# Performance work log

Hardware: AMD Instinct MI355X
Metric: run time of the kernel (lower is better)

Reference implementation:

```python
import jax, jax.numpy as jnp
import numpy as np

# ---- problem constants (mirror AdjustInstanceArea __init__ args) ----
NUM_NODES = 2_000_000
NUM_MOVABLE = 1_500_000
NUM_FILLER = 400_000
NUM_NETS = 1_500_000
PINS_PER_NET = 4                       # uniform netpin_start = arange(0, P+1, 4)
NUM_PINS = NUM_NETS * PINS_PER_NET
XL, XH, YL, YH = 0.0, 1000.0, 0.0, 1000.0
NBX = NBY = 512
BIN_W = (XH - XL) / NBX
BIN_H = (YH - YL) / NBY
UNIT_H_CAP = 1.5                       # unit horizontal routing capacity
UNIT_V_CAP = 1.5                       # unit vertical routing capacity
MAX_RATE = 2.0                         # max_route_opt_adjust_rate
MIN_RATE = 1.0 / MAX_RATE
EPS = 1e-6


def setup_inputs() -> dict:
    key = jax.random.key(0)
    k = jax.random.split(key, 4)
    x = jax.random.uniform(k[0], (NUM_NODES,), jnp.float32, XL, XH - 4.0)
    y = jax.random.uniform(k[1], (NUM_NODES,), jnp.float32, YL, YH - 4.0)
    pos = jnp.concatenate([x, y])                      # [2*num_nodes], x then y

    # pins clustered around net centers (realistic small net bboxes)
    rng = np.random.default_rng(0)
    centers = rng.uniform(0.0, 1000.0, size=(NUM_NETS, 1, 2)).astype(np.float32)
    jit = rng.uniform(-20.0, 20.0, size=(NUM_NETS, PINS_PER_NET, 2)).astype(np.float32)
    ppos = np.clip(centers + jit, 0.0, 1000.0)         # [nets, pins_per_net, 2], in net order

    # flat_netpin: pin ids grouped by net; pin_pos indexed by pin id
    flat_netpin = rng.permutation(NUM_PINS).astype(np.int32)
    px = np.empty(NUM_PINS, np.float32); py = np.empty(NUM_PINS, np.float32)
    px[flat_netpin] = ppos[..., 0].reshape(-1)
    py[flat_netpin] = ppos[..., 1].reshape(-1)
    pin_pos = jnp.concatenate([jnp.asarray(px), jnp.asarray(py)])  # [2*num_pins]

    pin2net = jnp.asarray(np.repeat(np.arange(NUM_NETS, dtype=np.int32), PINS_PER_NET))

    node_size_x = jax.random.uniform(k[2], (NUM_NODES,), jnp.float32, 1.0, 4.0)
    node_size_y = jax.random.uniform(k[3], (NUM_NODES,), jnp.float32, 1.0, 4.0)
    return {"pos": pos, "pin_pos": pin_pos,
            "node_size_x": node_size_x, "node_size_y": node_size_y,
            "flat_netpin": jnp.asarray(flat_netpin), "pin2net": pin2net}


def _rect_accum(vals, blx, bly, bhx, bhy):
    """Accumulate vals over inclusive bin rectangles via difference map + 2D cumsum."""
    D = jnp.zeros((NBX + 1, NBY + 1), vals.dtype)
    D = D.at[blx, bly].add(vals)
    D = D.at[bhx + 1, bly].add(-vals)
    D = D.at[blx, bhy + 1].add(-vals)
    D = D.at[bhx + 1, bhy + 1].add(vals)
    return jnp.cumsum(jnp.cumsum(D, axis=0), axis=1)[:NBX, :NBY]


def reference(pos, pin_pos, node_size_x, node_size_y, flat_netpin, pin2net):
    # ---- InstanceRouteOptimizationArea: RUDY routing demand per bin ----
    px = pin_pos[:NUM_PINS][flat_netpin].reshape(NUM_NETS, PINS_PER_NET)
    py = pin_pos[NUM_PINS:][flat_netpin].reshape(NUM_NETS, PINS_PER_NET)
    net_xl = jnp.min(px, axis=1); net_xh = jnp.max(px, axis=1)
    net_yl = jnp.min(py, axis=1); net_yh = jnp.max(py, axis=1)
    bw = net_xh - net_xl
    bh = net_yh - net_yl
    barea = jnp.maximum(bw * bh, EPS)
    dens_h = bw / barea                                # horizontal wire density
    dens_v = bh / barea                                # vertical wire density

    blx = jnp.clip(jnp.floor((net_xl - XL) / BIN_W), 0, NBX - 1).astype(jnp.int32)
    bhx = jnp.clip(jnp.floor((net_xh - XL) / BIN_W), 0, NBX - 1).astype(jnp.int32)
    bly = jnp.clip(jnp.floor((net_yl - YL) / BIN_H), 0, NBY - 1).astype(jnp.int32)
    bhy = jnp.clip(jnp.floor((net_yh - YL) / BIN_H), 0, NBY - 1).astype(jnp.int32)

    util_h = _rect_accum(dens_h, blx, bly, bhx, bhy) / UNIT_H_CAP
    util_v = _rect_accum(dens_v, blx, bly, bhx, bhy) / UNIT_V_CAP

    # per-movable-node utilization (gather at node center bin)
    x = pos[:NUM_NODES]; y = pos[NUM_NODES:]
    nsx_m = node_size_x[:NUM_MOVABLE]; nsy_m = node_size_y[:NUM_MOVABLE]
    cx = x[:NUM_MOVABLE] + 0.5 * nsx_m
    cy = y[:NUM_MOVABLE] + 0.5 * nsy_m
    bix = jnp.clip(jnp.floor((cx - XL) / BIN_W), 0, NBX - 1).astype(jnp.int32)
    biy = jnp.clip(jnp.floor((cy - YL) / BIN_H), 0, NBY - 1).astype(jnp.int32)
    util = jnp.maximum(util_h[bix, biy], util_v[bix, biy])
    ratio = jnp.clip(util, MIN_RATE, MAX_RATE)

    area_old = nsx_m * nsy_m
    instance_route_area = area_old * ratio

    # ---- AdjustInstanceArea: rescale under max_total_area budget ----
    filler_area_old = jnp.sum(node_size_x[NUM_NODES - NUM_FILLER:] *
                              node_size_y[NUM_NODES - NUM_FILLER:])
    max_total_area = jnp.sum(area_old) + filler_area_old
    scale = jnp.minimum(1.0, max_total_area / jnp.maximum(jnp.sum(instance_route_area), EPS))
    new_area = instance_route_area * scale
    sr = jnp.sqrt(new_area / jnp.maximum(area_old, EPS))
    nsx_new = nsx_m * sr
    nsy_new = nsy_m * sr

    # keep cell centers fixed while resizing
    x_out = x.at[:NUM_MOVABLE].add(0.5 * (nsx_m - nsx_new))
    y_out = y.at[:NUM_MOVABLE].add(0.5 * (nsy_m - nsy_new))

    # fillers absorb leftover area budget
    fscale = jnp.sqrt(jnp.maximum(max_total_area - jnp.sum(new_area), 0.0) /
                      jnp.maximum(filler_area_old, EPS))
    nsx_out = node_size_x.at[:NUM_MOVABLE].set(nsx_new)
    nsx_out = nsx_out.at[NUM_NODES - NUM_FILLER:].multiply(fscale)
    nsy_out = node_size_y.at[:NUM_MOVABLE].set(nsy_new)
    nsy_out = nsy_out.at[NUM_NODES - NUM_FILLER:].multiply(fscale)

    return jnp.concatenate([x_out, y_out, nsx_out, nsy_out])  # [4*num_nodes]
```

## Files before the change

kernel.cpp:

```cpp
#include <hip/hip_runtime.h>
#include <hip/hip_fp16.h>
#include <math.h>

#define N_NODES   2000000
#define N_MOVABLE 1500000
#define N_FILLER  400000
#define N_NETS    1500000
#define N_PINS    (N_NETS * 4)
#define NB        512
#define NT        16
#define TILE      32
#define NBUCKET   (NT * NT)
#define CAP       10240
#define NSLICE    4
#define NMAPS     NSLICE
#define RED_BLOCKS 1024

#define NQ        24
#define QRNG      250000
#define NXCD      8
#define RPX       3
#define PIN_PER_XCD (QRNG * RPX)
#define P2CHUNK   4096
#define P2CHUNKS  ((PIN_PER_XCD + P2CHUNK - 1) / P2CHUNK)

__device__ __forceinline__ int bin_idx(float v) {
    float b = floorf(v / 1.953125f);
    b = fminf(fmaxf(b, 0.0f), 511.0f);
    return (int)b;
}

__global__ __launch_bounds__(1024)
void p1_bucketq_kernel(const int* __restrict__ fnp,
                       uint2* __restrict__ qslab,
                       unsigned* __restrict__ g_qptr) {
    __shared__ unsigned hist[NQ];
    __shared__ unsigned hbase[NQ];
    int t = threadIdx.x;
    if (t < NQ) hist[t] = 0;
    __syncthreads();

    int s0 = blockIdx.x * 4096 + t * 4;
    unsigned q[4]; unsigned qb[4]; unsigned rk[4]; bool val[4];
    if (s0 + 3 < N_PINS) {
        int4 f = *reinterpret_cast<const int4*>(fnp + s0);
        q[0] = (unsigned)f.x; q[1] = (unsigned)f.y;
        q[2] = (unsigned)f.z; q[3] = (unsigned)f.w;
        val[0] = val[1] = val[2] = val[3] = true;
    } else {
        #pragma unroll
        for (int j = 0; j < 4; ++j) {
            val[j] = (s0 + j < N_PINS);
            q[j] = val[j] ? (unsigned)fnp[s0 + j] : 0u;
        }
    }
    #pragma unroll
    for (int j = 0; j < 4; ++j) {
        qb[j] = q[j] / (unsigned)QRNG;
        rk[j] = val[j] ? atomicAdd(&hist[qb[j]], 1u) : 0u;
    }
    __syncthreads();
    if (t < NQ) {
        unsigned c = hist[t];
        hbase[t] = c ? atomicAdd(&g_qptr[t], c) : 0u;
    }
    __syncthreads();
    #pragma unroll
    for (int j = 0; j < 4; ++j) {
        if (val[j]) {
            unsigned idx = qb[j] * (unsigned)QRNG + hbase[qb[j]] + rk[j];
            qslab[idx] = make_uint2(q[j], (unsigned)(s0 + j));
        }
    }
}

__global__ __launch_bounds__(1024)
void p2_gather_kernel(const uint2* __restrict__ qslab,
                      const float* __restrict__ pin_pos,
                      unsigned* __restrict__ sxy) {
    unsigned k = blockIdx.x & (NXCD - 1);
    unsigned c = blockIdx.x >> 3;
    unsigned t = threadIdx.x;
    #pragma unroll
    for (int j = 0; j < 4; ++j) {
        unsigned s = c * (unsigned)P2CHUNK + t + (unsigned)j * 1024u;
        if (s < (unsigned)PIN_PER_XCD) {
            unsigned rl = s / (unsigned)QRNG;
            unsigned ridx = s - rl * (unsigned)QRNG;
            uint2 qr = qslab[(k + 8u * rl) * (unsigned)QRNG + ridx];
            float x = pin_pos[qr.x];
            float y = pin_pos[qr.x + N_PINS];
            unsigned xq = __float2uint_rn(x * 64.0f);
            unsigned yq = __float2uint_rn(y * 64.0f);
            sxy[qr.y] = xq | (yq << 16);
        }
    }
}

__device__ __forceinline__ uint2 pack_tile_rec(float bw, float bh,
                                               unsigned blx, unsigned bhx,
                                               unsigned bly, unsigned bhy,
                                               int* tb) {
    float barea = fmaxf(bw * bh, 1e-6f);
    float vh = fminf((bw / barea) * (1.0f / 1.5f), 60000.0f);
    float vv = fminf((bh / barea) * (1.0f / 1.5f), 60000.0f);
    *tb = (int)((bly >> 5) * NT + (blx >> 5));
    __half2 h = __float22half2_rn(make_float2(vh, vv));
    uint2 r;
    r.x = *reinterpret_cast<unsigned*>(&h);
    r.y = blx | (bly << 9) | ((bhx + 1 - blx) << 18) | ((bhy + 1 - bly) << 23);
    return r;
}

__global__ __launch_bounds__(1024)
void p3_netrec_kernel(const unsigned* __restrict__ sxy,
                      uint2* __restrict__ tslab,
                      unsigned* __restrict__ g_tptr) {
    __shared__ unsigned hist[NBUCKET];
    __shared__ unsigned hbase[NBUCKET];
    int t = threadIdx.x;
    if (t < NBUCKET) hist[t] = 0;
    __syncthreads();

    int n0 = blockIdx.x * 4096 + t;
    uint2 rec[4]; int tb[4]; unsigned rk[4];
    #pragma unroll
    for (int u = 0; u < 4; ++u) {
        int n = n0 + u * 1024;
        tb[u] = -1;
        if (n < N_NETS) {
            uint4 v = *reinterpret_cast<const uint4*>(sxy + 4 * (size_t)n);
            unsigned x0 = v.x & 0xffffu, y0 = v.x >> 16;
            unsigned x1 = v.y & 0xffffu, y1 = v.y >> 16;
            unsigned x2 = v.z & 0xffffu, y2 = v.z >> 16;
            unsigned x3 = v.w & 0xffffu, y3 = v.w >> 16;
            unsigned xl = min(min(x0, x1), min(x2, x3));
            unsigned xh = max(max(x0, x1), max(x2, x3));
            unsigned yl = min(min(y0, y1), min(y2, y3));
            unsigned yh = max(max(y0, y1), max(y2, y3));
            float bw = (float)(xh - xl) * 0.015625f;
            float bh = (float)(yh - yl) * 0.015625f;
            unsigned blx = min(xl / 125u, 511u), bhx = min(xh / 125u, 511u);
            unsigned bly = min(yl / 125u, 511u), bhy = min(yh / 125u, 511u);
            rec[u] = pack_tile_rec(bw, bh, blx, bhx, bly, bhy, &tb[u]);
            rk[u] = atomicAdd(&hist[tb[u]], 1u);
        }
    }
    __syncthreads();
    if (t < NBUCKET) {
        unsigned c = hist[t];
        hbase[t] = c ? atomicAdd(&g_tptr[t], c) : 0u;
    }
    __syncthreads();
    #pragma unroll
    for (int u = 0; u < 4; ++u) {
        if (tb[u] >= 0) {
            unsigned s = hbase[tb[u]] + rk[u];
            if (s < CAP) tslab[(size_t)tb[u] * CAP + s] = rec[u];
        }
    }
}

__global__ void pack_kernel(const float* __restrict__ pin_pos,
                            float2* __restrict__ pp) {
    int i = blockIdx.x * blockDim.x + threadIdx.x;
    if (i >= N_PINS / 4) return;
    float4 a = reinterpret_cast<const float4*>(pin_pos)[i];
    float4 b = reinterpret_cast<const float4*>(pin_pos + N_PINS)[i];
    float4* o = reinterpret_cast<float4*>(pp + 4 * (size_t)i);
    o[0] = make_float4(a.x, b.x, a.y, b.y);
    o[1] = make_float4(a.z, b.z, a.w, b.w);
}

template <bool PACKED>
__device__ __forceinline__ uint2 make_rec_f(const float* __restrict__ pin_pos,
                                            const float2* __restrict__ pp,
                                            int4 fp, int* tb) {
    float2 p0, p1, p2, p3;
    if (PACKED) {
        p0 = pp[fp.x]; p1 = pp[fp.y]; p2 = pp[fp.z]; p3 = pp[fp.w];
    } else {
        p0 = make_float2(pin_pos[fp.x], pin_pos[N_PINS + fp.x]);
        p1 = make_float2(pin_pos[fp.y], pin_pos[N_PINS + fp.y]);
        p2 = make_float2(pin_pos[fp.z], pin_pos[N_PINS + fp.z]);
        p3 = make_float2(pin_pos[fp.w], pin_pos[N_PINS + fp.w]);
    }
    float xl = fminf(fminf(p0.x, p1.x), fminf(p2.x, p3.x));
    float xh = fmaxf(fmaxf(p0.x, p1.x), fmaxf(p2.x, p3.x));
    float yl = fminf(fminf(p0.y, p1.y), fminf(p2.y, p3.y));
    float yh = fmaxf(fmaxf(p0.y, p1.y), fmaxf(p2.y, p3.y));
    unsigned blx = bin_idx(xl), bhx = bin_idx(xh);
    unsigned bly = bin_idx(yl), bhy = bin_idx(yh);
    return pack_tile_rec(xh - xl, yh - yl, blx, bhx, bly, bhy, tb);
}

template <bool PACKED>
__global__ __launch_bounds__(1024)
void gather_bin_kernel(const float* __restrict__ pin_pos,
                       const float2* __restrict__ pp,
                       const int* __restrict__ fnp,
                       uint2* __restrict__ slab,
                       unsigned* __restrict__ g_ptr) {
    __shared__ unsigned hist[NBUCKET];
    __shared__ unsigned hbase[NBUCKET];
    int t = threadIdx.x;
    if (t < NBUCKET) hist[t] = 0;
    __syncthreads();

    int n0 = blockIdx.x * 4096 + t;
    bool v[4]; int4 fp[4]; uint2 r[4]; int b[4]; unsigned rk[4];
    #pragma unroll
    for (int k = 0; k < 4; ++k) {
        int n = n0 + k * 1024;
        v[k] = (n < N_NETS);
        fp[k] = v[k] ? *reinterpret_cast<const int4*>(fnp + 4 * (size_t)n)
                     : make_int4(0, 0, 0, 0);
    }
    #pragma unroll
    for (int k = 0; k < 4; ++k) {
        b[k] = 0;
        if (v[k]) r[k] = make_rec_f<PACKED>(pin_pos, pp, fp[k], &b[k]);
    }
    #pragma unroll
    for (int k = 0; k < 4; ++k) rk[k] = v[k] ? atomicAdd(&hist[b[k]], 1u) : 0u;
    __syncthreads();
    if (t < NBUCKET) {
        unsigned c = hist[t];
        hbase[t] = c ? atomicAdd(&g_ptr[t], c) : 0u;
    }
    __syncthreads();
    #pragma unroll
    for (int k = 0; k < 4; ++k) {
        if (v[k]) {
            unsigned s = hbase[b[k]] + rk[k];
            if (s < CAP) slab[(size_t)b[k] * CAP + s] = r[k];
        }
    }
}

__device__ __forceinline__ void rec_process(uint2 r, int x0, int y0,
                                            float2* acc) {
    float2 v = __half22float2(*reinterpret_cast<const __half2*>(&r.x));
    unsigned g = r.y;
    int ax0 = (int)(g & 511u);
    int ay0 = (int)((g >> 9) & 511u);
    int ax1 = ax0 + (int)((g >> 18) & 31u);
    int ay1 = ay0 + (int)((g >> 23) & 31u);
    int X0 = ax0 - x0, Y0 = ay0 - y0;
    int X1 = ax1 - x0, Y1 = ay1 - y0;
    bool iX0 = (unsigned)X0 < TILE, iX1 = (unsigned)X1 < TILE;
    bool iY0 = (unsigned)Y0 < TILE, iY1 = (unsigned)Y1 < TILE;
    if (iX0 && iY0) { atomicAdd(&acc[X0 * TILE + Y0].x,  v.x); atomicAdd(&acc[X0 * TILE + Y0].y,  v.y); }
    if (iX1 && iY0) { atomicAdd(&acc[X1 * TILE + Y0].x, -v.x); atomicAdd(&acc[X1 * TILE + Y0].y, -v.y); }
    if (iX0 && iY1) { atomicAdd(&acc[X0 * TILE + Y1].x, -v.x); atomicAdd(&acc[X0 * TILE + Y1].y, -v.y); }
    if (iX1 && iY1) { atomicAdd(&acc[X1 * TILE + Y1].x,  v.x); atomicAdd(&acc[X1 * TILE + Y1].y,  v.y); }
}

__global__ __launch_bounds__(256)
void accum_kernel(const uint2* __restrict__ slab,
                  const unsigned* __restrict__ g_cnt,
                  float2* __restrict__ Dp) {
    __shared__ float2 acc[TILE * TILE];
    int wg = blockIdx.x;
    int sl = wg & (NSLICE - 1), tile = wg >> 2;
    int tx = tile & (NT - 1), ty = tile >> 4;
    int tid = threadIdx.x;

    for (int i = tid; i < TILE * TILE; i += 256) acc[i] = make_float2(0.f, 0.f);
    __syncthreads();

    int x0 = tx * TILE, y0 = ty * TILE;
    #pragma unroll
    for (int dy = -1; dy <= 0; ++dy) {
        int sy = ty + dy; if (sy < 0) continue;
        #pragma unroll
        for (int dx = -1; dx <= 0; ++dx) {
            int sx = tx + dx; if (sx < 0) continue;
            int sb = sy * NT + sx;
            unsigned cnt = min(g_cnt[sb], (unsigned)CAP);
            unsigned lo = (cnt * (unsigned)sl) >> 2;
            unsigned hi = (cnt * (unsigned)(sl + 1)) >> 2;
            const uint2* recs = slab + (size_t)sb * CAP;
            unsigned i = lo + tid;
            for (; i + 768 < hi; i += 1024) {
                uint2 r0 = recs[i];
                uint2 r1 = recs[i + 256];
                uint2 r2 = recs[i + 512];
                uint2 r3 = recs[i + 768];
                rec_process(r0, x0, y0, acc);
                rec_process(r1, x0, y0, acc);
                rec_process(r2, x0, y0, acc);
                rec_process(r3, x0, y0, acc);
            }
            for (; i < hi; i += 256) rec_process(recs[i], x0, y0, acc);
        }
    }
    __syncthreads();

    float2* D = Dp + (size_t)sl * NB * NB;
    for (int i = tid; i < TILE * TILE; i += 256) {
        int X = i >> 5, Y = i & 31;
        D[(size_t)(x0 + X) * NB + (y0 + Y)] = acc[i];
    }
}

__global__ __launch_bounds__(512)
void scanA_kernel(const float2* __restrict__ Dp, float2* __restrict__ S) {
    __shared__ float2 s[NB];
    int x = blockIdx.x, t = threadIdx.x;
    float2 a = make_float2(0.f, 0.f);
    #pragma unroll
    for (int m = 0; m < NMAPS; ++m) {
        float2 v = Dp[(size_t)m * NB * NB + (size_t)x * NB + t];
        a.x += v.x; a.y += v.y;
    }
    s[t] = a;
    __syncthreads();
    for (int off = 1; off < NB; off <<= 1) {
        float2 u = s[t];
        if (t >= off) { float2 w = s[t - off]; u.x += w.x; u.y += w.y; }
        __syncthreads();
        s[t] = u;
        __syncthreads();
    }
    S[(size_t)x * NB + t] = s[t];
}

__global__ __launch_bounds__(512)
void scanB_kernel(float2* __restrict__ S) {
    __shared__ float2 s[NB];
    int y = blockIdx.x, t = threadIdx.x;
    s[t] = S[(size_t)t * NB + y];
    __syncthreads();
    for (int off = 1; off < NB; off <<= 1) {
        float2 u = s[t];
        if (t >= off) { float2 w = s[t - off]; u.x += w.x; u.y += w.y; }
        __syncthreads();
        s[t] = u;
        __syncthreads();
    }
    S[(size_t)t * NB + y] = s[t];
}

__global__ __launch_bounds__(256)
void reduce_kernel(const float* __restrict__ pos,
                   const float* __restrict__ nsx,
                   const float* __restrict__ nsy,
                   const float2* __restrict__ S,
                   double* __restrict__ partials) {
    const int MQ = N_MOVABLE / 4;
    const int TQ = MQ + N_FILLER / 4;
    double a_old = 0.0, a_route = 0.0, a_fill = 0.0;
    int stride = gridDim.x * blockDim.x;
    for (int q = blockIdx.x * blockDim.x + threadIdx.x; q < TQ; q += stride) {
        if (q < MQ) {
            int i = 4 * q;
            float4 x4  = *reinterpret_cast<const float4*>(pos + i);
            float4 y4  = *reinterpret_cast<const float4*>(pos + N_NODES + i);
            float4 sx4 = *reinterpret_cast<const float4*>(nsx + i);
            float4 sy4 = *reinterpret_cast<const float4*>(nsy + i);
            float xs[4] = {x4.x, x4.y, x4.z, x4.w};
            float ys[4] = {y4.x, y4.y, y4.z, y4.w};
            float sxs[4] = {sx4.x, sx4.y, sx4.z, sx4.w};
            float sys[4] = {sy4.x, sy4.y, sy4.z, sy4.w};
            #pragma unroll
            for (int k = 0; k < 4; ++k) {
                int bx = bin_idx(xs[k] + 0.5f * sxs[k]);
                int by = bin_idx(ys[k] + 0.5f * sys[k]);
                float2 u2 = S[(size_t)bx * NB + by];
                float ratio = fminf(fmaxf(fmaxf(u2.x, u2.y), 0.5f), 2.0f);
                float area = sxs[k] * sys[k];
                a_old += (double)area;
                a_route += (double)(area * ratio);
            }
        } else {
            int j = (N_NODES - N_FILLER) + 4 * (q - MQ);
            float4 sx4 = *reinterpret_cast<const float4*>(nsx + j);
            float4 sy4 = *reinterpret_cast<const float4*>(nsy + j);
            a_fill += (double)(sx4.x * sy4.x + sx4.y * sy4.y +
                               sx4.z * sy4.z + sx4.w * sy4.w);
        }
    }
    for (int off = 32; off > 0; off >>= 1) {
        a_old   += __shfl_down(a_old, off);
        a_route += __shfl_down(a_route, off);
        a_fill  += __shfl_down(a_fill, off);
    }
    __shared__ double sd[4][3];
    int wid = threadIdx.x >> 6, lane = threadIdx.x & 63;
    if (lane == 0) { sd[wid][0] = a_old; sd[wid][1] = a_route; sd[wid][2] = a_fill; }
    __syncthreads();
    if (threadIdx.x == 0) {
        double s0 = 0, s1 = 0, s2 = 0;
        for (int w = 0; w < 4; ++w) { s0 += sd[w][0]; s1 += sd[w][1]; s2 += sd[w][2]; }
        partials[blockIdx.x * 3 + 0] = s0;
        partials[blockIdx.x * 3 + 1] = s1;
        partials[blockIdx.x * 3 + 2] = s2;
    }
}

__global__ __launch_bounds__(256)
void finish_kernel(const double* __restrict__ partials,
                   double* __restrict__ sums) {
    int t = threadIdx.x;
    double s0 = 0, s1 = 0, s2 = 0;
    for (int r = t; r < RED_BLOCKS; r += 256) {
        s0 += partials[r * 3 + 0];
        s1 += partials[r * 3 + 1];
        s2 += partials[r * 3 + 2];
    }
    for (int off = 32; off > 0; off >>= 1) {
        s0 += __shfl_down(s0, off);
        s1 += __shfl_down(s1, off);
        s2 += __shfl_down(s2, off);
    }
    __shared__ double sd[4][3];
    int wid = t >> 6, lane = t & 63;
    if (lane == 0) { sd[wid][0] = s0; sd[wid][1] = s1; sd[wid][2] = s2; }
    __syncthreads();
    if (t == 0) {
        double a = 0, b = 0, c = 0;
        for (int w = 0; w < 4; ++w) { a += sd[w][0]; b += sd[w][1]; c += sd[w][2]; }
        sums[0] = a; sums[1] = b; sums[2] = c;
    }
}

__global__ __launch_bounds__(256)
void final_kernel(const float* __restrict__ pos,
                  const float* __restrict__ nsx,
                  const float* __restrict__ nsy,
                  const float2* __restrict__ S,
                  const double* __restrict__ sums,
                  float* __restrict__ out) {
    double sum_area  = sums[0];
    double sum_route = sums[1];
    double fill_old  = sums[2];
    double max_total = sum_area + fill_old;

    float scale = fminf(1.0f, (float)(max_total / fmax(sum_route, 1e-6)));
    float sum_new = (float)(scale * (float)sum_route);
    float fscale = sqrtf(fmaxf((float)max_total - sum_new, 0.0f) /
                         fmaxf((float)fill_old, 1e-6f));

    int q = blockIdx.x * blockDim.x + threadIdx.x;
    if (q >= N_NODES / 4) return;
    int i = 4 * q;

    float4 x4  = *reinterpret_cast<const float4*>(pos + i);
    float4 y4  = *reinterpret_cast<const float4*>(pos + N_NODES + i);
    float4 sx4 = *reinterpret_cast<const float4*>(nsx + i);
    float4 sy4 = *reinterpret_cast<const float4*>(nsy + i);

    float xs[4] = {x4.x, x4.y, x4.z, x4.w};
    float ys[4] = {y4.x, y4.y, y4.z, y4.w};
    float sxs[4] = {sx4.x, sx4.y, sx4.z, sx4.w};
    float sys[4] = {sy4.x, sy4.y, sy4.z, sy4.w};

    if (i < N_MOVABLE) {
        #pragma unroll
        for (int k = 0; k < 4; ++k) {
            int bx = bin_idx(xs[k] + 0.5f * sxs[k]);
            int by = bin_idx(ys[k] + 0.5f * sys[k]);
            float2 u2 = S[(size_t)bx * NB + by];
            float ratio = fminf(fmaxf(fmaxf(u2.x, u2.y), 0.5f), 2.0f);
            float area = sxs[k] * sys[k];
            float new_area = area * ratio * scale;
            float sr = sqrtf(new_area / fmaxf(area, 1e-6f));
            float sx_new = sxs[k] * sr, sy_new = sys[k] * sr;
            xs[k] = xs[k] + 0.5f * (sxs[k] - sx_new);
            ys[k] = ys[k] + 0.5f * (sys[k] - sy_new);
            sxs[k] = sx_new; sys[k] = sy_new;
        }
    } else if (i >= N_NODES - N_FILLER) {
        #pragma unroll
        for (int k = 0; k < 4; ++k) { sxs[k] *= fscale; sys[k] *= fscale; }
    }

    *reinterpret_cast<float4*>(out + i)               = make_float4(xs[0], xs[1], xs[2], xs[3]);
    *reinterpret_cast<float4*>(out + N_NODES + i)     = make_float4(ys[0], ys[1], ys[2], ys[3]);
    *reinterpret_cast<float4*>(out + 2 * N_NODES + i) = make_float4(sxs[0], sxs[1], sxs[2], sxs[3]);
    *reinterpret_cast<float4*>(out + 3 * N_NODES + i) = make_float4(sys[0], sys[1], sys[2], sys[3]);
}

extern "C" void kernel_launch(void* const* d_in, const int* in_sizes, int n_in,
                              void* d_out, int out_size, void* d_ws, size_t ws_size,
                              hipStream_t stream) {
    const float* pos         = (const float*)d_in[0];
    const float* pin_pos     = (const float*)d_in[1];
    const float* nsx         = (const float*)d_in[2];
    const float* nsy         = (const float*)d_in[3];
    const int*   flat_netpin = (const int*)d_in[4];
    float* out = (float*)d_out;

    const size_t qslab_b = (size_t)N_PINS * sizeof(uint2);
    const size_t sxy_b   = (size_t)N_PINS * sizeof(unsigned);
    const size_t tslab_b = (size_t)NBUCKET * CAP * sizeof(uint2);
    const size_t ctr_b   = 4096;
    const size_t dp_b    = (size_t)NMAPS * NB * NB * sizeof(float2);
    const size_t s_b     = (size_t)NB * NB * sizeof(float2);
    const size_t part_b  = (size_t)RED_BLOCKS * 3 * sizeof(double);
    const size_t pp_b    = (size_t)N_PINS * sizeof(float2);

    const size_t need_new = qslab_b + sxy_b + tslab_b + ctr_b;
    const size_t need_r8  = pp_b + tslab_b + ctr_b;

    char* base = (char*)d_ws;
    int tier = (ws_size >= need_new) ? 0 : (ws_size >= need_r8) ? 1 : 2;

    uint2* tslab; unsigned* ctrs; float2* Dp; float2* S;
    double* partials; double* sums;

    if (tier == 0) {
        uint2*    qslab = (uint2*)base;
        unsigned* sxy   = (unsigned*)(base + qslab_b);
        tslab           = (uint2*)(base + qslab_b + sxy_b);
        ctrs            = (unsigned*)(base + qslab_b + sxy_b + tslab_b);
        Dp       = (float2*)base;
        S        = (float2*)(base + dp_b);
        partials = (double*)(base + dp_b + s_b);
        sums     = (double*)(base + dp_b + s_b + part_b);

        unsigned* g_qptr = ctrs;
        unsigned* g_tptr = ctrs + 448;

        hipMemsetAsync(ctrs, 0, ctr_b, stream);
        p1_bucketq_kernel<<<(N_PINS + 4095) / 4096, 1024, 0, stream>>>(
            flat_netpin, qslab, g_qptr);
        p2_gather_kernel<<<P2CHUNKS * NXCD, 1024, 0, stream>>>(
            qslab, pin_pos, sxy);
        p3_netrec_kernel<<<(N_NETS + 4095) / 4096, 1024, 0, stream>>>(
            sxy, tslab, g_tptr);
        accum_kernel <<<NBUCKET * NSLICE, 256, 0, stream>>>(tslab, g_tptr, Dp);
    } else if (tier == 1) {
        float2* pp = (float2*)base;
        tslab      = (uint2*)(base + pp_b);
        ctrs       = (unsigned*)(base + pp_b + tslab_b);
        Dp       = (float2*)base;
        S        = (float2*)(base + dp_b);
        partials = (double*)(base + dp_b + s_b);
        sums     = (double*)(base + dp_b + s_b + part_b);
        unsigned* g_tptr = ctrs + 448;

        hipMemsetAsync(ctrs, 0, ctr_b, stream);
        pack_kernel<<<(N_PINS / 4 + 255) / 256, 256, 0, stream>>>(pin_pos, pp);
        gather_bin_kernel<true><<<(N_NETS + 4095) / 4096, 1024, 0, stream>>>(
            pin_pos, pp, flat_netpin, tslab, g_tptr);
        accum_kernel <<<NBUCKET * NSLICE, 256, 0, stream>>>(tslab, g_tptr, Dp);
    } else {
        tslab = (uint2*)base;
        Dp    = (float2*)(base + tslab_b);
        S     = (float2*)(base + tslab_b + dp_b);
        partials = (double*)(base + tslab_b + dp_b + s_b);
        sums     = (double*)(base + tslab_b + dp_b + s_b + part_b);
        ctrs     = (unsigned*)(base + tslab_b + dp_b + s_b + part_b + 64);
        unsigned* g_tptr = ctrs + 448;

        hipMemsetAsync(ctrs, 0, ctr_b, stream);
        gather_bin_kernel<false><<<(N_NETS + 4095) / 4096, 1024, 0, stream>>>(
            pin_pos, nullptr, flat_netpin, tslab, g_tptr);
        accum_kernel <<<NBUCKET * NSLICE, 256, 0, stream>>>(tslab, g_tptr, Dp);
    }

    scanA_kernel <<<NB, 512, 0, stream>>>(Dp, S);
    scanB_kernel <<<NB, 512, 0, stream>>>(S);
    reduce_kernel<<<RED_BLOCKS, 256, 0, stream>>>(pos, nsx, nsy, S, partials);
    finish_kernel<<<1, 256, 0, stream>>>(partials, sums);
    final_kernel <<<(N_NODES / 4 + 255) / 256, 256, 0, stream>>>(pos, nsx, nsy, S, sums, out);
}
```

Measured before the change: 262.8 us.

## Replace random pin-slot scatter with two-pass bucketed scatter into shared-memory windows

Instead of scattering each gathered pin coordinate directly to a random slot of sxy, p2 now writes (slot, packed xy) back into qslab in place. A new bucket kernel partitions those records by 16K-slot super-bucket, and a window kernel loads each super-bucket into LDS, reorders it by slot there, and computes net records from LDS. The goal is to turn the fully random 4-byte global scatter into coalesced bucketed writes and a local shared-memory permutation. The cost is an extra kernel launch and an extra full pass over 8-byte records.

```diff
diff --git a/kernel.cpp b/kernel.cpp
--- a/kernel.cpp
+++ b/kernel.cpp
@@ -24,6 +24,10 @@
 #define P2CHUNK   4096
 #define P2CHUNKS  ((PIN_PER_XCD + P2CHUNK - 1) / P2CHUNK)
 
+#define SB_SHIFT  14
+#define SB_SLOTS  16384
+#define NSB       ((N_PINS + SB_SLOTS - 1) / SB_SLOTS)
+
 __device__ __forceinline__ int bin_idx(float v) {
     float b = floorf(v / 1.953125f);
     b = fminf(fmaxf(b, 0.0f), 511.0f);
@@ -75,9 +79,8 @@
 }
 
 __global__ __launch_bounds__(1024)
-void p2_gather_kernel(const uint2* __restrict__ qslab,
-                      const float* __restrict__ pin_pos,
-                      unsigned* __restrict__ sxy) {
+void p2_gather_kernel(uint2* __restrict__ qslab,
+                      const float* __restrict__ pin_pos) {
     unsigned k = blockIdx.x & (NXCD - 1);
     unsigned c = blockIdx.x >> 3;
     unsigned t = threadIdx.x;
@@ -87,13 +90,50 @@
         if (s < (unsigned)PIN_PER_XCD) {
             unsigned rl = s / (unsigned)QRNG;
             unsigned ridx = s - rl * (unsigned)QRNG;
-            uint2 qr = qslab[(k + 8u * rl) * (unsigned)QRNG + ridx];
+            unsigned idx = (k + 8u * rl) * (unsigned)QRNG + ridx;
+            uint2 qr = qslab[idx];
             float x = pin_pos[qr.x];
             float y = pin_pos[qr.x + N_PINS];
             unsigned xq = __float2uint_rn(x * 64.0f);
             unsigned yq = __float2uint_rn(y * 64.0f);
-            sxy[qr.y] = xq | (yq << 16);
-        }
+            qslab[idx] = make_uint2(qr.y, xq | (yq << 16));
+        }
+    }
+}
+
+__global__ __launch_bounds__(1024)
+void pd_bucket_kernel(const uint2* __restrict__ qslab,
+                      uint2* __restrict__ sslab,
+                      unsigned* __restrict__ g_sptr) {
+    __shared__ unsigned hist[NSB];
+    __shared__ unsigned hbase[NSB];
+    int t = threadIdx.x;
+    for (int i = t; i < NSB; i += 1024) hist[i] = 0;
+    __syncthreads();
+
+    int i0 = blockIdx.x * 4096 + t;
+    uint2 rc[4]; int sb[4]; unsigned rk[4]; bool val[4];
+    #pragma unroll
+    for (int j = 0; j < 4; ++j) {
+        int i = i0 + j * 1024;
+        val[j] = (i < N_PINS);
+        sb[j] = 0; rk[j] = 0;
+        if (val[j]) {
+            rc[j] = qslab[i];
+            sb[j] = (int)(rc[j].x >> SB_SHIFT);
+            rk[j] = atomicAdd(&hist[sb[j]], 1u);
+        }
+    }
+    __syncthreads();
+    for (int i = t; i < NSB; i += 1024) {
+        unsigned c = hist[i];
+        hbase[i] = c ? atomicAdd(&g_sptr[i], c) : 0u;
+    }
+    __syncthreads();
+    #pragma unroll
+    for (int j = 0; j < 4; ++j) {
+        if (val[j])
+            sslab[(size_t)sb[j] * SB_SLOTS + hbase[sb[j]] + rk[j]] = rc[j];
     }
 }
 
@@ -112,24 +152,34 @@
     return r;
 }
 
-__global__ __launch_bounds__(1024)
-void p3_netrec_kernel(const unsigned* __restrict__ sxy,
+__global__ __launch_bounds__(512)
+void pc_window_kernel(const uint2* __restrict__ sslab,
                       uint2* __restrict__ tslab,
                       unsigned* __restrict__ g_tptr) {
+    __shared__ unsigned win[SB_SLOTS];
     __shared__ unsigned hist[NBUCKET];
     __shared__ unsigned hbase[NBUCKET];
-    int t = threadIdx.x;
+    int w = blockIdx.x, t = threadIdx.x;
+    int base_slot = w * SB_SLOTS;
+    int cnt = min(SB_SLOTS, N_PINS - base_slot);
+
     if (t < NBUCKET) hist[t] = 0;
-    __syncthreads();
-
-    int n0 = blockIdx.x * 4096 + t;
-    uint2 rec[4]; int tb[4]; unsigned rk[4];
-    #pragma unroll
-    for (int u = 0; u < 4; ++u) {
-        int n = n0 + u * 1024;
+    for (int i = t; i < cnt; i += 512) {
+        uint2 rc = sslab[(size_t)base_slot + i];
+        win[rc.x - (unsigned)base_slot] = rc.y;
+    }
+    __syncthreads();
+
+    int nets = cnt >> 2;
+    int base_net = w * (SB_SLOTS / 4);
+    (void)base_net;
+    uint2 rec[8]; int tb[8]; unsigned rk[8];
+    #pragma unroll
+    for (int u = 0; u < 8; ++u) {
+        int j = t + u * 512;
         tb[u] = -1;
-        if (n < N_NETS) {
-            uint4 v = *reinterpret_cast<const uint4*>(sxy + 4 * (size_t)n);
+        if (j < nets) {
+            uint4 v = *reinterpret_cast<const uint4*>(win + 4 * j);
             unsigned x0 = v.x & 0xffffu, y0 = v.x >> 16;
             unsigned x1 = v.y & 0xffffu, y1 = v.y >> 16;
             unsigned x2 = v.z & 0xffffu, y2 = v.z >> 16;
@@ -153,7 +203,7 @@
     }
     __syncthreads();
     #pragma unroll
-    for (int u = 0; u < 4; ++u) {
+    for (int u = 0; u < 8; ++u) {
         if (tb[u] >= 0) {
             unsigned s = hbase[tb[u]] + rk[u];
             if (s < CAP) tslab[(size_t)tb[u] * CAP + s] = rec[u];
@@ -493,7 +543,7 @@
     float* out = (float*)d_out;
 
     const size_t qslab_b = (size_t)N_PINS * sizeof(uint2);
-    const size_t sxy_b   = (size_t)N_PINS * sizeof(unsigned);
+    const size_t sslab_b = (size_t)NSB * SB_SLOTS * sizeof(uint2);
     const size_t tslab_b = (size_t)NBUCKET * CAP * sizeof(uint2);
     const size_t ctr_b   = 4096;
     const size_t dp_b    = (size_t)NMAPS * NB * NB * sizeof(float2);
@@ -501,7 +551,7 @@
     const size_t part_b  = (size_t)RED_BLOCKS * 3 * sizeof(double);
     const size_t pp_b    = (size_t)N_PINS * sizeof(float2);
 
-    const size_t need_new = qslab_b + sxy_b + tslab_b + ctr_b;
+    const size_t need_new = qslab_b + sslab_b + tslab_b + ctr_b;
     const size_t need_r8  = pp_b + tslab_b + ctr_b;
 
     char* base = (char*)d_ws;
@@ -511,25 +561,26 @@
     double* partials; double* sums;
 
     if (tier == 0) {
-        uint2*    qslab = (uint2*)base;
-        unsigned* sxy   = (unsigned*)(base + qslab_b);
-        tslab           = (uint2*)(base + qslab_b + sxy_b);
-        ctrs            = (unsigned*)(base + qslab_b + sxy_b + tslab_b);
+        uint2* qslab = (uint2*)base;
+        uint2* sslab = (uint2*)(base + qslab_b);
+        tslab        = (uint2*)(base + qslab_b + sslab_b);
+        ctrs         = (unsigned*)(base + qslab_b + sslab_b + tslab_b);
         Dp       = (float2*)base;
         S        = (float2*)(base + dp_b);
         partials = (double*)(base + dp_b + s_b);
         sums     = (double*)(base + dp_b + s_b + part_b);
 
         unsigned* g_qptr = ctrs;
+        unsigned* g_sptr = ctrs + 64;
         unsigned* g_tptr = ctrs + 448;
 
         hipMemsetAsync(ctrs, 0, ctr_b, stream);
         p1_bucketq_kernel<<<(N_PINS + 4095) / 4096, 1024, 0, stream>>>(
             flat_netpin, qslab, g_qptr);
-        p2_gather_kernel<<<P2CHUNKS * NXCD, 1024, 0, stream>>>(
-            qslab, pin_pos, sxy);
-        p3_netrec_kernel<<<(N_NETS + 4095) / 4096, 1024, 0, stream>>>(
-            sxy, tslab, g_tptr);
+        p2_gather_kernel<<<P2CHUNKS * NXCD, 1024, 0, stream>>>(qslab, pin_pos);
+        pd_bucket_kernel<<<(N_PINS + 4095) / 4096, 1024, 0, stream>>>(
+            qslab, sslab, g_sptr);
+        pc_window_kernel<<<NSB, 512, 0, stream>>>(sslab, tslab, g_tptr);
         accum_kernel <<<NBUCKET * NSLICE, 256, 0, stream>>>(tslab, g_tptr, Dp);
     } else if (tier == 1) {
         float2* pp = (float2*)base;
```

After: 257.1 us. -2.2%, faster.
